# Kernel optimization log

Measured on AMD Instinct MI355X. Metric: run time of the kernel, lower is better.

Reference implementation:

```python
import jax, jax.numpy as jnp
import numpy as np
from jax import lax

LAMBDA_OBJ = 5.0
LAMBDA_NOOBJ = 1.0
LAMBDA_PRIOR = 0.01
LAMBDA_COORD = 1.0
IOU_THRESHOLD = 0.6
PRIOR_SEEN_THRESHOLD = 12800


def _cxcywh_to_xyxy(b):
    cx, cy, w, h = b[..., 0], b[..., 1], b[..., 2], b[..., 3]
    return jnp.stack([cx - w / 2, cy - h / 2, cx + w / 2, cy + h / 2], -1)


def _box_iou(a, b):
    # a: (N,4), b: (M,4), xyxy -> (N,M)
    lt = jnp.maximum(a[:, None, :2], b[None, :, :2])
    rb = jnp.minimum(a[:, None, 2:], b[None, :, 2:])
    wh = jnp.clip(rb - lt, 0.0)
    inter = wh[..., 0] * wh[..., 1]
    area_a = (a[:, 2] - a[:, 0]) * (a[:, 3] - a[:, 1])
    area_b = (b[:, 2] - b[:, 0]) * (b[:, 3] - b[:, 1])
    return inter / (area_a[:, None] + area_b[None, :] - inter)


def setup_inputs() -> dict:
    key = jax.random.key(0)
    B, A, C, GY, GX, N = 64, 5, 80, 32, 32, 50
    ks = jax.random.split(key, 6)
    pred = jax.random.normal(ks[0], (B, A * (5 + C), GY, GX), jnp.float32) * 0.1
    dxdy = jax.random.uniform(ks[1], (B, N, 2))  # offset within cell, sigmoid-space target
    gx = jax.random.randint(ks[2], (B, N, 1), 0, GX).astype(jnp.float32)
    gy = jax.random.randint(ks[3], (B, N, 1), 0, GY).astype(jnp.float32)
    wh = jax.random.uniform(ks[4], (B, N, 2), minval=0.05, maxval=0.95)  # positive for log
    cl = jax.random.randint(ks[5], (B, N, 1), 0, C).astype(jnp.float32)
    gt_batch = jnp.concatenate([dxdy, gx, gy, wh, cl], -1)  # (B,N,7): dx,dy,gx,gy,w,h,c
    base = np.array([[1.3, 1.69], [3.19, 4.0], [5.05, 8.09], [9.47, 4.84], [11.2, 10.0]],
                    np.float32) / 32.0  # normalized YOLOv2 anchors
    anchors = jnp.asarray(base).reshape(1, A, 2, 1, 1)
    return {"pred": pred, "gt_batch": gt_batch, "anchors": anchors, "seen": 0}


def _loss(pred, gt_batch, anchors, seen):
    B, channel, GY, GX = pred.shape
    A = anchors.shape[1]
    ch = channel // A
    C = ch - 5
    num_boxes = A * GY * GX

    p = pred.reshape(B, A, ch, GY, GX)
    p = jnp.concatenate([
        jax.nn.sigmoid(p[:, :, :2]),        # dx, dy
        p[:, :, 2:4],                        # raw tw, th
        jax.nn.sigmoid(p[:, :, 4:5]),        # objectness
        jax.nn.softmax(p[:, :, 5:], axis=2), # class probs
    ], axis=2)
    anc = anchors[0, :, :, 0, 0]  # (A,2)

    # ---- matching (torch.no_grad equivalent) ----
    g = lax.stop_gradient(gt_batch)   # (B,N,7)
    pm = lax.stop_gradient(p)
    anc_ng = lax.stop_gradient(anc)

    gwh = g[..., 4:6]  # (B,N,2)
    inter = jnp.minimum(gwh[:, :, None, :], anc_ng[None, None]).prod(-1)  # (B,N,A)
    aiou = inter / (gwh.prod(-1)[..., None] + anc_ng.prod(-1)[None, None] - inter)
    best_prior = jnp.argmax(aiou, -1)  # (B,N)
    gxi = g[..., 2].astype(jnp.int32)
    gyi = g[..., 3].astype(jnp.int32)
    best_box = best_prior * GX * GY + gyi * GX + gxi  # (B,N), index into a*H*W+h*W+w

    gt_boxes = _cxcywh_to_xyxy(jnp.concatenate([
        (g[..., 0] + g[..., 2] / GX)[..., None],
        (g[..., 1] + g[..., 3] / GY)[..., None],
        gwh,
    ], -1))  # (B,N,4)

    grid = jnp.stack([
        jnp.broadcast_to((jnp.arange(GX, dtype=jnp.float32) / GX)[None, :], (GY, GX)),
        jnp.broadcast_to((jnp.arange(GY, dtype=jnp.float32) / GY)[:, None], (GY, GX)),
    ], 0)  # (2,GY,GX) corner offsets
    pcxcy = pm[:, :, :2] + grid[None, None]
    pwh = anc_ng[None, :, :, None, None] * jnp.exp(pm[:, :, 2:4])
    pboxes = jnp.concatenate([pcxcy, pwh], 2).transpose(0, 1, 3, 4, 2).reshape(B, num_boxes, 4)
    pboxes = _cxcywh_to_xyxy(pboxes)

    pred_iou = jax.vmap(_box_iou)(gt_boxes, pboxes)  # (B,N,num_boxes)
    best_gt_overlap = pred_iou.max(1)                # (B,num_boxes)
    pos = jnp.where(best_gt_overlap > IOU_THRESHOLD, 2.0, 0.0)
    pos = jax.vmap(lambda pv, idx: pv.at[idx].set(1.0))(pos, best_box)

    enc = jnp.concatenate([g[..., 0:2], jnp.log(gwh) - jnp.log(anc_ng[best_prior])], -1)  # (B,N,4)
    iou_t = jnp.take_along_axis(pred_iou, best_box[:, :, None], axis=2)[..., 0]           # (B,N)
    gidx = (best_box + jnp.arange(B, dtype=best_box.dtype)[:, None] * num_boxes).reshape(-1)

    # ---- loss terms ----
    pf = p.transpose(0, 1, 3, 4, 2).reshape(-1, ch)  # (B*num_boxes, ch)
    posf = pos.reshape(-1)

    noobj = jnp.sum(jnp.where(posf == 0, pf[:, 4] ** 2, 0.0))

    if seen < PRIOR_SEEN_THRESHOLD:  # seen is a static Python int
        truth = jnp.array([0.5 / GX, 0.5 / GY, 0.0, 0.0], pf.dtype)
        prior = jnp.sum(jnp.where((posf != 1)[:, None], (pf[:, :4] - truth) ** 2, 0.0))
    else:
        prior = jnp.asarray(0.0, pf.dtype)

    gp = pf[gidx]  # (B*N, ch)
    coord = jnp.sum((gp[:, :4] - enc.reshape(-1, 4)) ** 2)
    obj = jnp.sum((gp[:, 4] - iou_t.reshape(-1)) ** 2)
    onehot = jax.nn.one_hot(g[..., 6].astype(jnp.int32).reshape(-1), C, dtype=pf.dtype)
    cls = jnp.sum((gp[:, 5:] - onehot) ** 2)

    return (cls + LAMBDA_NOOBJ * noobj + LAMBDA_OBJ * obj
            + LAMBDA_COORD * coord + LAMBDA_PRIOR * prior)


def reference(pred, gt_batch, anchors, seen):
    return _loss(pred, gt_batch, anchors, seen)
```

## Files before the change

### kernel.cpp

```cpp
#include <hip/hip_runtime.h>
#include <math.h>

#define B_    64
#define A_    5
#define C_    80
#define GY_   32
#define GX_   32
#define N_    50
#define CH_   85
#define PLANE_ 1024
#define NBLK_ (B_ * A_ * 4)

__device__ __forceinline__ float sigmoidf_(float x) {
    return 1.0f / (1.0f + __expf(-x));
}

__device__ __forceinline__ float waveReduceSum(float v) {
    #pragma unroll
    for (int m = 32; m >= 1; m >>= 1) v += __shfl_xor(v, m, 64);
    return v;
}

__device__ __forceinline__ float waveReduceMax(float v) {
    #pragma unroll
    for (int m = 32; m >= 1; m >>= 1) v = fmaxf(v, __shfl_xor(v, m, 64));
    return v;
}

__global__ __launch_bounds__(256) void yolo_fused(
        const float* __restrict__ pred, const float* __restrict__ gt,
        const float* __restrict__ anc, const int* __restrict__ seen,
        float* __restrict__ partial) {
    __shared__ float4 sgt[N_];
    __shared__ float4 senc[N_];
    __shared__ int    sbb[N_];
    __shared__ int    scls[N_];

    int bid = blockIdx.x;
    int b = bid / 20; int r = bid - b * 20;
    int a = r >> 2; int chunk = r & 3;
    int tid = threadIdx.x;

    if (tid < N_) {
        const float* g = gt + (b * N_ + tid) * 7;
        float dx = g[0], dy = g[1], gxf = g[2], gyf = g[3], gw = g[4], gh = g[5];
        float best = -1.0f; int bp = 0;
        #pragma unroll
        for (int aa = 0; aa < A_; aa++) {
            float aw = anc[2 * aa], ah = anc[2 * aa + 1];
            float inter = fminf(gw, aw) * fminf(gh, ah);
            float iou = inter / (gw * gh + aw * ah - inter);
            if (iou > best) { best = iou; bp = aa; }
        }
        sbb[tid] = bp * PLANE_ + (int)gyf * GX_ + (int)gxf;
        float cx = dx + gxf / (float)GX_;
        float cy = dy + gyf / (float)GY_;
        sgt[tid]  = make_float4(cx - gw * 0.5f, cy - gh * 0.5f,
                                cx + gw * 0.5f, cy + gh * 0.5f);
        senc[tid] = make_float4(dx, dy, __logf(gw) - __logf(anc[2 * bp]),
                                        __logf(gh) - __logf(anc[2 * bp + 1]));
        scls[tid] = (int)g[6];
    }
    __syncthreads();

    int spatial = chunk * 256 + tid;
    int gy = spatial >> 5, gx = spatial & 31;
    const float* p = pred + (size_t)(b * A_ + a) * CH_ * PLANE_ + spatial;
    float tx = p[0], ty = p[PLANE_], tw = p[2 * PLANE_],
          th = p[3 * PLANE_], to = p[4 * PLANE_];
    float sx = sigmoidf_(tx), sy = sigmoidf_(ty), so = sigmoidf_(to);

    float pcx = sx + (float)gx / (float)GX_;
    float pcy = sy + (float)gy / (float)GY_;
    float pw = anc[2 * a] * __expf(tw);
    float ph = anc[2 * a + 1] * __expf(th);
    float px1 = pcx - pw * 0.5f, py1 = pcy - ph * 0.5f;
    float px2 = pcx + pw * 0.5f, py2 = pcy + ph * 0.5f;
    float areap = pw * ph;

    int myIdx = a * PLANE_ + spatial;
    float maxIou = 0.0f;
    bool isBest = false;
    for (int n = 0; n < N_; n++) {
        float4 gb = sgt[n];
        float ix = fmaxf(fminf(gb.z, px2) - fmaxf(gb.x, px1), 0.0f);
        float iy = fmaxf(fminf(gb.w, py2) - fmaxf(gb.y, py1), 0.0f);
        float inter = ix * iy;
        float areag = (gb.z - gb.x) * (gb.w - gb.y);
        float iou = inter / (areag + areap - inter);
        maxIou = fmaxf(maxIou, iou);
        isBest = isBest || (sbb[n] == myIdx);
    }

    float acc = (!isBest && !(maxIou > 0.6f)) ? so * so : 0.0f;
    if (seen[0] < 12800 && !isBest) {
        float d0 = sx - 0.015625f, d1 = sy - 0.015625f;
        acc += 0.01f * (d0 * d0 + d1 * d1 + tw * tw + th * th);
    }

    int lane = tid & 63;
    for (int n = 0; n < N_; n++) {
        int bbn = sbb[n];
        bool own = (bbn == myIdx);
        unsigned long long mask = __ballot(own);
        if (mask == 0ULL) continue;
        int owner = (int)__ffsll((long long)mask) - 1;
        int sp = __shfl(spatial, owner, 64);

        float z1 = p[(5 + lane) * PLANE_ + (sp - spatial)];
        float z2 = (lane < 16) ? p[(69 + lane) * PLANE_ + (sp - spatial)] : -1e30f;
        float m = waveReduceMax(fmaxf(z1, z2));
        float e1 = __expf(z1 - m);
        float e2 = (lane < 16) ? __expf(z2 - m) : 0.0f;
        float S = waveReduceSum(e1 + e2);
        float inv = 1.0f / S;

        int cls = scls[n];
        float s1 = e1 * inv;
        float d1 = s1 - ((lane == cls) ? 1.0f : 0.0f);
        float term = d1 * d1;
        if (lane < 16) {
            float s2 = e2 * inv;
            float d2 = s2 - (((64 + lane) == cls) ? 1.0f : 0.0f);
            term += d2 * d2;
        }
        float clsSum = waveReduceSum(term);

        if (own) {
            float4 gb = sgt[n];
            float ix = fmaxf(fminf(gb.z, px2) - fmaxf(gb.x, px1), 0.0f);
            float iy = fmaxf(fminf(gb.w, py2) - fmaxf(gb.y, py1), 0.0f);
            float inter = ix * iy;
            float areag = (gb.z - gb.x) * (gb.w - gb.y);
            float iou_t = inter / (areag + areap - inter);

            float4 e = senc[n];
            float c0 = sx - e.x, c1 = sy - e.y, c2 = tw - e.z, c3 = th - e.w;
            float coord = c0 * c0 + c1 * c1 + c2 * c2 + c3 * c3;
            float ot = so - iou_t;
            acc += clsSum + coord + 5.0f * ot * ot;
        }
    }

    acc = waveReduceSum(acc);
    __shared__ float part[4];
    if (lane == 0) part[tid >> 6] = acc;
    __syncthreads();
    if (tid == 0) partial[bid] = part[0] + part[1] + part[2] + part[3];
}

__global__ __launch_bounds__(256) void yolo_reduce(
        const float* __restrict__ partial, float* __restrict__ out) {
    int tid = threadIdx.x;
    float v = 0.0f;
    #pragma unroll
    for (int i = 0; i < 5; i++) v += partial[tid + 256 * i];
    v = waveReduceSum(v);
    __shared__ float part[4];
    if ((tid & 63) == 0) part[tid >> 6] = v;
    __syncthreads();
    if (tid == 0) out[0] = part[0] + part[1] + part[2] + part[3];
}

extern "C" void kernel_launch(void* const* d_in, const int* in_sizes, int n_in,
                              void* d_out, int out_size, void* d_ws, size_t ws_size,
                              hipStream_t stream) {
    const float* pred = (const float*)d_in[0];
    const float* gt   = (const float*)d_in[1];
    const float* anc  = (const float*)d_in[2];
    const int*   seen = (const int*)d_in[3];
    float* out = (float*)d_out;
    float* partial = (float*)d_ws;

    yolo_fused<<<NBLK_, 256, 0, stream>>>(pred, gt, anc, seen, partial);
    yolo_reduce<<<1, 256, 0, stream>>>(partial, out);
}
```

Baseline: 165.9 us.

## Replace IoU division with threshold comparison and prefilter GT boxes per block

```diff
diff --git a/kernel.cpp b/kernel.cpp
--- a/kernel.cpp
+++ b/kernel.cpp
@@ -32,14 +32,19 @@
         const float* __restrict__ anc, const int* __restrict__ seen,
         float* __restrict__ partial) {
     __shared__ float4 sgt[N_];
+    __shared__ float  sga[N_];
     __shared__ float4 senc[N_];
     __shared__ int    sbb[N_];
     __shared__ int    scls[N_];
+    __shared__ int    slist[N_];
+    __shared__ int    scnt;
 
     int bid = blockIdx.x;
     int b = bid / 20; int r = bid - b * 20;
     int a = r >> 2; int chunk = r & 3;
     int tid = threadIdx.x;
+    if (tid == 0) scnt = 0;
+    __syncthreads();
 
     if (tid < N_) {
         const float* g = gt + (b * N_ + tid) * 7;
@@ -52,63 +57,65 @@
             float iou = inter / (gw * gh + aw * ah - inter);
             if (iou > best) { best = iou; bp = aa; }
         }
-        sbb[tid] = bp * PLANE_ + (int)gyf * GX_ + (int)gxf;
-        float cx = dx + gxf / (float)GX_;
-        float cy = dy + gyf / (float)GY_;
+        int bb = bp * PLANE_ + (int)gyf * GX_ + (int)gxf;
+        sbb[tid] = bb;
+        float cx = dx + gxf * (1.0f / 32.0f);
+        float cy = dy + gyf * (1.0f / 32.0f);
         sgt[tid]  = make_float4(cx - gw * 0.5f, cy - gh * 0.5f,
                                 cx + gw * 0.5f, cy + gh * 0.5f);
+        sga[tid]  = 0.375f * gw * gh;
         senc[tid] = make_float4(dx, dy, __logf(gw) - __logf(anc[2 * bp]),
                                         __logf(gh) - __logf(anc[2 * bp + 1]));
         scls[tid] = (int)g[6];
+        if ((bb >> 10) == a && ((bb & 1023) >> 8) == chunk) {
+            int slot = atomicAdd(&scnt, 1);
+            slist[slot] = tid;
+        }
     }
     __syncthreads();
 
     int spatial = chunk * 256 + tid;
     int gy = spatial >> 5, gx = spatial & 31;
-    const float* p = pred + (size_t)(b * A_ + a) * CH_ * PLANE_ + spatial;
+    const float* pb = pred + (size_t)(b * A_ + a) * (CH_ * PLANE_);
+    const float* p = pb + spatial;
     float tx = p[0], ty = p[PLANE_], tw = p[2 * PLANE_],
           th = p[3 * PLANE_], to = p[4 * PLANE_];
     float sx = sigmoidf_(tx), sy = sigmoidf_(ty), so = sigmoidf_(to);
 
-    float pcx = sx + (float)gx / (float)GX_;
-    float pcy = sy + (float)gy / (float)GY_;
+    float pcx = sx + (float)gx * (1.0f / 32.0f);
+    float pcy = sy + (float)gy * (1.0f / 32.0f);
     float pw = anc[2 * a] * __expf(tw);
     float ph = anc[2 * a + 1] * __expf(th);
     float px1 = pcx - pw * 0.5f, py1 = pcy - ph * 0.5f;
     float px2 = pcx + pw * 0.5f, py2 = pcy + ph * 0.5f;
     float areap = pw * ph;
+    float a375p = 0.375f * areap;
 
-    int myIdx = a * PLANE_ + spatial;
-    float maxIou = 0.0f;
-    bool isBest = false;
+    bool anyHigh = false;
+    #pragma unroll 10
     for (int n = 0; n < N_; n++) {
         float4 gb = sgt[n];
         float ix = fmaxf(fminf(gb.z, px2) - fmaxf(gb.x, px1), 0.0f);
         float iy = fmaxf(fminf(gb.w, py2) - fmaxf(gb.y, py1), 0.0f);
-        float inter = ix * iy;
-        float areag = (gb.z - gb.x) * (gb.w - gb.y);
-        float iou = inter / (areag + areap - inter);
-        maxIou = fmaxf(maxIou, iou);
-        isBest = isBest || (sbb[n] == myIdx);
-    }
-
-    float acc = (!isBest && !(maxIou > 0.6f)) ? so * so : 0.0f;
-    if (seen[0] < 12800 && !isBest) {
-        float d0 = sx - 0.015625f, d1 = sy - 0.015625f;
-        acc += 0.01f * (d0 * d0 + d1 * d1 + tw * tw + th * th);
+        anyHigh = anyHigh || (ix * iy > sga[n] + a375p);
     }
 
     int lane = tid & 63;
-    for (int n = 0; n < N_; n++) {
+    int myIdx = a * PLANE_ + spatial;
+    bool isBest = false;
+    float acc = 0.0f;
+    int cnt = scnt;
+    for (int i = 0; i < cnt; i++) {
+        int n = slist[i];
         int bbn = sbb[n];
         bool own = (bbn == myIdx);
+        isBest = isBest || own;
         unsigned long long mask = __ballot(own);
         if (mask == 0ULL) continue;
-        int owner = (int)__ffsll((long long)mask) - 1;
-        int sp = __shfl(spatial, owner, 64);
+        int sp = bbn & 1023;
 
-        float z1 = p[(5 + lane) * PLANE_ + (sp - spatial)];
-        float z2 = (lane < 16) ? p[(69 + lane) * PLANE_ + (sp - spatial)] : -1e30f;
+        float z1 = pb[(5 + lane) * PLANE_ + sp];
+        float z2 = (lane < 16) ? pb[(69 + lane) * PLANE_ + sp] : -1e30f;
         float m = waveReduceMax(fmaxf(z1, z2));
         float e1 = __expf(z1 - m);
         float e2 = (lane < 16) ? __expf(z2 - m) : 0.0f;
@@ -116,12 +123,10 @@
         float inv = 1.0f / S;
 
         int cls = scls[n];
-        float s1 = e1 * inv;
-        float d1 = s1 - ((lane == cls) ? 1.0f : 0.0f);
+        float d1 = e1 * inv - ((lane == cls) ? 1.0f : 0.0f);
         float term = d1 * d1;
         if (lane < 16) {
-            float s2 = e2 * inv;
-            float d2 = s2 - (((64 + lane) == cls) ? 1.0f : 0.0f);
+            float d2 = e2 * inv - (((64 + lane) == cls) ? 1.0f : 0.0f);
             term += d2 * d2;
         }
         float clsSum = waveReduceSum(term);
@@ -136,9 +141,17 @@
 
             float4 e = senc[n];
             float c0 = sx - e.x, c1 = sy - e.y, c2 = tw - e.z, c3 = th - e.w;
-            float coord = c0 * c0 + c1 * c1 + c2 * c2 + c3 * c3;
             float ot = so - iou_t;
-            acc += clsSum + coord + 5.0f * ot * ot;
+            acc += clsSum + c0 * c0 + c1 * c1 + c2 * c2 + c3 * c3
+                 + 5.0f * ot * ot;
+        }
+    }
+
+    if (!isBest) {
+        if (!anyHigh) acc += so * so;
+        if (seen[0] < 12800) {
+            float d0 = sx - 0.015625f, d1 = sy - 0.015625f;
+            acc += 0.01f * (d0 * d0 + d1 * d1 + tw * tw + th * th);
         }
     }
 
```

Result: faster. 161.7 us (-2.6%).
